# Optimization experiments

Hardware: AMD Instinct MI355X
Metric: run time of the kernel (lower is better)

The kernel has to match this reference:

```python
import jax, jax.numpy as jnp
import numpy as np

E = 8            # moe_num_experts
HIDDEN = 1024    # hidden_size
FFN = 4096       # ffn_hidden_size
TOKENS = 8192    # total tokens, pre-sorted by expert; balanced -> TOKENS // E per expert


def setup_inputs() -> dict:
    key = jax.random.key(0)
    k1, k2, k3 = jax.random.split(key, 3)
    x = jax.random.normal(k1, (TOKENS, HIDDEN), dtype=jnp.float32)
    # w1, w2 stored flattened as [E*FFN, HIDDEN], matching create_dmoe_expert_weights' view([-1, columns])
    w1 = jax.random.normal(k2, (E * FFN, HIDDEN), dtype=jnp.float32) * (1.0 / np.sqrt(HIDDEN))
    w2 = jax.random.normal(k3, (E * FFN, HIDDEN), dtype=jnp.float32) * (1.0 / np.sqrt(FFN))
    return {"x": x, "w1": w1, "w2": w2, "num_experts": E}


def reference(x, w1, w2, num_experts):
    # Block-diagonal topology of dMoE SparseMLP: tokens sorted by expert, each
    # expert owns a contiguous FFN slice of w1/w2. Equivalent grouped GEMM:
    #   out_e = gelu(x_e @ w1_e^T) @ w2_e   (megablocks gelu = tanh-approx GELU)
    tokens, hidden = x.shape
    ffn = w1.shape[0] // num_experts
    tpe = tokens // num_experts  # tokens per expert (balanced topology)
    xe = x.reshape(num_experts, tpe, hidden)        # [E, T/E, H]
    w1e = w1.reshape(num_experts, ffn, hidden)      # [E, F, H]
    w2e = w2.reshape(num_experts, ffn, hidden)      # [E, F, H]
    h = jax.nn.gelu(jnp.einsum('eth,efh->etf', xe, w1e), approximate=True)  # sdd + gelu
    out = jnp.einsum('etf,efh->eth', h, w2e)        # dsd
    return out.reshape(tokens, hidden)
```

## Files before the change

kernel.cpp:

```cpp
#include <hip/hip_runtime.h>
#include <hip/hip_bf16.h>
#include <stdint.h>

#define NE 8
#define HID 1024
#define FFN 4096
#define TOK 8192
#define TPE (TOK / NE)

typedef __attribute__((ext_vector_type(8))) short    bf16x8;
typedef __attribute__((ext_vector_type(4))) float    f32x4;
typedef __attribute__((ext_vector_type(4))) unsigned short ushort4v;
typedef __attribute__((ext_vector_type(8))) unsigned short ushort8v;


__device__ __forceinline__ unsigned short f2bf(float f) {
    union { float f; unsigned u; } c; c.f = f;
    unsigned r = c.u + 0x7fffu + ((c.u >> 16) & 1u);
    return (unsigned short)(r >> 16);
}

__device__ __forceinline__ float gelu_tanh(float x) {
    const float c0 = 0.7978845608028654f;
    const float c1 = 0.044715f;
    float u = c0 * (x + c1 * x * x * x);
    float t = 1.0f - 2.0f / (1.0f + __expf(2.0f * u));
    return 0.5f * x * (1.0f + t);
}

typedef const __attribute__((address_space(1))) void gbl_void_t;
typedef __attribute__((address_space(3))) void lds_void_t;

__device__ __forceinline__ void gload_lds16(const void* g, void* l) {
    __builtin_amdgcn_global_load_lds((gbl_void_t*)g, (lds_void_t*)l, 16, 0, 0);
}


__global__ void cvt_f32_bf16(const float* __restrict__ in,
                             unsigned short* __restrict__ out) {
    size_t i = ((size_t)blockIdx.x * blockDim.x + threadIdx.x) * 8;
    f32x4 a = *(const f32x4*)(in + i);
    f32x4 b = *(const f32x4*)(in + i + 4);
    ushort8v o;
#pragma unroll
    for (int j = 0; j < 4; j++) { o[j] = f2bf(a[j]); o[4 + j] = f2bf(b[j]); }
    *(ushort8v*)(out + i) = o;
}


__global__ void transpose_cvt(const float* __restrict__ in,
                              unsigned short* __restrict__ out) {
    __shared__ unsigned short tile[64][65];
    const int e  = blockIdx.z;
    const int f0 = blockIdx.x * 64;
    const int h0 = blockIdx.y * 64;
    const float*     src = in  + (size_t)e * FFN * HID;
    unsigned short*  dst = out + (size_t)e * HID * FFN;
    const int t  = threadIdx.x;
    const int tr = t >> 4;
    const int tc = (t & 15) * 4;
#pragma unroll
    for (int i = 0; i < 4; i++) {
        int f = i * 16 + tr;
        f32x4 v = *(const f32x4*)(src + (size_t)(f0 + f) * HID + h0 + tc);
#pragma unroll
        for (int j = 0; j < 4; j++) tile[f][tc + j] = f2bf(v[j]);
    }
    __syncthreads();
#pragma unroll
    for (int i = 0; i < 4; i++) {
        int h = i * 16 + tr;
        ushort4v o;
#pragma unroll
        for (int j = 0; j < 4; j++) o[j] = tile[tc + j][h];
        *(ushort4v*)(dst + (size_t)(h0 + h) * FFN + f0 + tc) = o;
    }
}


template <int BN, bool GELU>
__global__ __launch_bounds__(512, 2)
void gemm8p(const unsigned short* __restrict__ A,
            const unsigned short* __restrict__ B,
            void* __restrict__ Cout, int M, int N, int K) {
    constexpr int BM = 256, BK = 64;
    constexpr int NI = BN / 64;
    constexpr int NH = NI / 2;
    constexpr int ABYTES = BM * BK * 2;
    constexpr int BBYTES = BN * BK * 2;
    constexpr int BUF = ABYTES + BBYTES;
    constexpr int LPTA = ABYTES / (512 * 16);
    constexpr int LPTB = BBYTES / (512 * 16);
    constexpr int LPT = LPTA + LPTB;

    __shared__ __align__(16) char lds[2 * BUF];

    const int e  = blockIdx.z;
    const int m0 = blockIdx.x * BM;
    const int n0 = blockIdx.y * BN;
    const unsigned short* Ae = A + (size_t)e * M * K;
    const unsigned short* Be = B + (size_t)e * N * K;

    const int tid  = threadIdx.x;
    const int lane = tid & 63;
    const int w    = tid >> 6;
    const int wr   = w >> 2;
    const int wc   = w & 3;
    const int fr   = lane & 15;
    const int fq   = lane >> 4;
    const int swz  = (lane & 7) << 4;
    const int kx0  = (fq * 16) ^ swz;
    const int kx1  = (64 + fq * 16) ^ swz;
    const int aoff = (wr * 128 + fr) * 128;
    const int boff = ABYTES + (wc * (BN / 4) + fr) * 128;

    const unsigned short* asrc[LPTA];
    const unsigned short* bsrc[LPTB];
    int adst[LPTA], bdst[LPTB];
#pragma unroll
    for (int i = 0; i < LPTA; i++) {
        int c = tid + 512 * i; int row = c >> 3; int kb = (c & 7) << 4;
        int kbs = kb ^ ((row & 7) << 4);
        asrc[i] = Ae + (size_t)(m0 + row) * K + (kbs >> 1);
        adst[i] = c * 16;
    }
#pragma unroll
    for (int i = 0; i < LPTB; i++) {
        int c = tid + 512 * i; int row = c >> 3; int kb = (c & 7) << 4;
        int kbs = kb ^ ((row & 7) << 4);
        bsrc[i] = Be + (size_t)(n0 + row) * K + (kbs >> 1);
        bdst[i] = ABYTES + c * 16;
    }

    auto STAGE = [&](int it) {
        char* base = lds + (it & 1) * BUF;
        const int kt = it * BK;
#pragma unroll
        for (int i = 0; i < LPTA; i++) gload_lds16(asrc[i] + kt, base + adst[i]);
#pragma unroll
        for (int i = 0; i < LPTB; i++) gload_lds16(bsrc[i] + kt, base + bdst[i]);
    };

    f32x4 acc[8][NI];
#pragma unroll
    for (int i = 0; i < 8; i++)
#pragma unroll
        for (int j = 0; j < NI; j++) acc[i][j] = f32x4{0.f, 0.f, 0.f, 0.f};

    bf16x8 a[4][2], b[NH][2];
    const char* pa = nullptr; const char* pb = nullptr;

    auto LDA = [&](int mh) {
#pragma unroll
        for (int mi = 0; mi < 4; mi++) {
            a[mi][0] = *(const bf16x8*)(pa + mh * 8192 + mi * 2048 + kx0);
            a[mi][1] = *(const bf16x8*)(pa + mh * 8192 + mi * 2048 + kx1);
        }
    };
    auto LDB = [&](int nh) {
#pragma unroll
        for (int ni = 0; ni < NH; ni++) {
            b[ni][0] = *(const bf16x8*)(pb + nh * (NH * 2048) + ni * 2048 + kx0);
            b[ni][1] = *(const bf16x8*)(pb + nh * (NH * 2048) + ni * 2048 + kx1);
        }
    };
    auto MM = [&](int mh, int nh) {
        __builtin_amdgcn_s_setprio(1);
#pragma unroll
        for (int mi = 0; mi < 4; mi++)
#pragma unroll
            for (int ni = 0; ni < NH; ni++) {
                acc[mh * 4 + mi][nh * NH + ni] = __builtin_amdgcn_mfma_f32_16x16x32_bf16(
                    a[mi][0], b[ni][0], acc[mh * 4 + mi][nh * NH + ni], 0, 0, 0);
                acc[mh * 4 + mi][nh * NH + ni] = __builtin_amdgcn_mfma_f32_16x16x32_bf16(
                    a[mi][1], b[ni][1], acc[mh * 4 + mi][nh * NH + ni], 0, 0, 0);
            }
        __builtin_amdgcn_s_setprio(0);
    };

    STAGE(0); STAGE(1);
    if constexpr (LPT == 8) asm volatile("s_waitcnt vmcnt(8)" ::: "memory");
    else                    asm volatile("s_waitcnt vmcnt(6)" ::: "memory");
    __builtin_amdgcn_sched_barrier(0);
    __builtin_amdgcn_s_barrier();
    __builtin_amdgcn_sched_barrier(0);

    const int NT = K / BK;
    for (int it = 0; it < NT; ++it) {
        const char* bb = lds + (it & 1) * BUF;
        pa = bb + aoff; pb = bb + boff;
        LDA(0); LDB(0); MM(0, 0);
        LDB(1);         MM(0, 1);
        LDA(1);         MM(1, 1);
        LDB(0);         MM(1, 0);
        __builtin_amdgcn_sched_barrier(0);
        __builtin_amdgcn_s_barrier();
        __builtin_amdgcn_sched_barrier(0);
        if (it + 2 < NT) {
            STAGE(it + 2);
            if constexpr (LPT == 8) asm volatile("s_waitcnt vmcnt(8)" ::: "memory");
            else                    asm volatile("s_waitcnt vmcnt(6)" ::: "memory");
        } else {
            asm volatile("s_waitcnt vmcnt(0)" ::: "memory");
        }
        __builtin_amdgcn_sched_barrier(0);
        __builtin_amdgcn_s_barrier();
        __builtin_amdgcn_sched_barrier(0);
    }

    const int r0 = m0 + wr * 128 + fq * 4;
    const int c0 = n0 + wc * (BN / 4) + fr;
    if constexpr (GELU) {
        unsigned short* C = (unsigned short*)Cout + (size_t)e * M * N;
#pragma unroll
        for (int mi = 0; mi < 8; mi++)
#pragma unroll
            for (int ni = 0; ni < NI; ni++) {
                int row = r0 + mi * 16, col = c0 + ni * 16;
#pragma unroll
                for (int r = 0; r < 4; r++)
                    C[(size_t)(row + r) * N + col] = f2bf(gelu_tanh(acc[mi][ni][r]));
            }
    } else {
        float* C = (float*)Cout + (size_t)e * M * N;
#pragma unroll
        for (int mi = 0; mi < 8; mi++)
#pragma unroll
            for (int ni = 0; ni < NI; ni++) {
                int row = r0 + mi * 16, col = c0 + ni * 16;
#pragma unroll
                for (int r = 0; r < 4; r++)
                    C[(size_t)(row + r) * N + col] = acc[mi][ni][r];
            }
    }
}


__global__ void fused_fallback(const float* __restrict__ x,
                               const float* __restrict__ w1,
                               const float* __restrict__ w2,
                               float* __restrict__ out) {
    __shared__ float xs[HID];
    __shared__ float hs[FFN];
    const int tok = blockIdx.x;
    const int e   = tok / TPE;
    const float* w1e = w1 + (size_t)e * FFN * HID;
    const float* w2e = w2 + (size_t)e * FFN * HID;
    const int t = threadIdx.x;
    for (int i = t; i < HID; i += 256) xs[i] = x[(size_t)tok * HID + i];
    __syncthreads();
    for (int f = t; f < FFN; f += 256) {
        const float* wr = w1e + (size_t)f * HID;
        float s = 0.f;
        for (int k = 0; k < HID; k++) s += xs[k] * wr[k];
        hs[f] = gelu_tanh(s);
    }
    __syncthreads();
    for (int h = t; h < HID; h += 256) {
        float s = 0.f;
        for (int f = 0; f < FFN; f++) s += hs[f] * w2e[(size_t)f * HID + h];
        out[(size_t)tok * HID + h] = s;
    }
}


extern "C" void kernel_launch(void* const* d_in, const int* in_sizes, int n_in,
                              void* d_out, int out_size, void* d_ws, size_t ws_size,
                              hipStream_t stream) {
    const float* x  = (const float*)d_in[0];
    const float* w1 = (const float*)d_in[1];
    const float* w2 = (const float*)d_in[2];
    float* out = (float*)d_out;

    const size_t XB  = (size_t)TOK * HID * 2;
    const size_t W1B = (size_t)NE * FFN * HID * 2;
    const size_t W2B = W1B;
    const size_t HB  = (size_t)TOK * FFN * 2;
    const size_t need = XB + W1B + W2B + HB;

    if (ws_size >= need) {
        char* ws = (char*)d_ws;
        unsigned short* xb  = (unsigned short*)ws;
        unsigned short* w1b = (unsigned short*)(ws + XB);
        unsigned short* w2t = (unsigned short*)(ws + XB + W1B);
        unsigned short* hb  = (unsigned short*)(ws + XB + W1B + W2B);

        cvt_f32_bf16<<<(TOK * HID) / (256 * 8), 256, 0, stream>>>(x, xb);
        cvt_f32_bf16<<<(NE * FFN * HID) / (256 * 8), 256, 0, stream>>>(w1, w1b);
        transpose_cvt<<<dim3(FFN / 64, HID / 64, NE), 256, 0, stream>>>(w2, w2t);

        gemm8p<256, true><<<dim3(TPE / 256, FFN / 256, NE), 512, 0, stream>>>(
            xb, w1b, hb, TPE, FFN, HID);
        gemm8p<128, false><<<dim3(TPE / 256, HID / 128, NE), 512, 0, stream>>>(
            hb, w2t, out, TPE, HID, FFN);
    } else {
        fused_fallback<<<TOK, 256, 0, stream>>>(x, w1, w2, out);
    }
}
```

Baseline: 259.1 us.

## Interleave split global-to-LDS loads with quarter MFMA phases in 8-wave GEMM

```diff
diff --git a/kernel.cpp b/kernel.cpp
--- a/kernel.cpp
+++ b/kernel.cpp
@@ -84,62 +84,63 @@
             const unsigned short* __restrict__ B,
             void* __restrict__ Cout, int M, int N, int K) {
     constexpr int BM = 256, BK = 64;
-    constexpr int NI = BN / 64;
-    constexpr int NH = NI / 2;
+    constexpr int NH = BN / 128;
+    constexpr int NI = 2 * NH;
+    constexpr int LB = BN / 128;
+    constexpr int S  = BN / 8;
     constexpr int ABYTES = BM * BK * 2;
     constexpr int BBYTES = BN * BK * 2;
     constexpr int BUF = ABYTES + BBYTES;
-    constexpr int LPTA = ABYTES / (512 * 16);
-    constexpr int LPTB = BBYTES / (512 * 16);
-    constexpr int LPT = LPTA + LPTB;
+    constexpr int VMC = 2 + 2 * LB;
 
     __shared__ __align__(16) char lds[2 * BUF];
 
     const int e  = blockIdx.z;
     const int m0 = blockIdx.x * BM;
     const int n0 = blockIdx.y * BN;
-    const unsigned short* Ae = A + (size_t)e * M * K;
-    const unsigned short* Be = B + (size_t)e * N * K;
+    const size_t K2 = (size_t)K * 2;
+    const char* Ae = (const char*)(A + (size_t)e * M * K);
+    const char* Be = (const char*)(B + (size_t)e * N * K);
 
     const int tid  = threadIdx.x;
     const int lane = tid & 63;
     const int w    = tid >> 6;
-    const int wr   = w >> 2;
-    const int wc   = w & 3;
-    const int fr   = lane & 15;
-    const int fq   = lane >> 4;
-    const int swz  = (lane & 7) << 4;
-    const int kx0  = (fq * 16) ^ swz;
-    const int kx1  = (64 + fq * 16) ^ swz;
-    const int aoff = (wr * 128 + fr) * 128;
-    const int boff = ABYTES + (wc * (BN / 4) + fr) * 128;
-
-    const unsigned short* asrc[LPTA];
-    const unsigned short* bsrc[LPTB];
-    int adst[LPTA], bdst[LPTB];
-#pragma unroll
-    for (int i = 0; i < LPTA; i++) {
-        int c = tid + 512 * i; int row = c >> 3; int kb = (c & 7) << 4;
-        int kbs = kb ^ ((row & 7) << 4);
-        asrc[i] = Ae + (size_t)(m0 + row) * K + (kbs >> 1);
-        adst[i] = c * 16;
-    }
-#pragma unroll
-    for (int i = 0; i < LPTB; i++) {
-        int c = tid + 512 * i; int row = c >> 3; int kb = (c & 7) << 4;
-        int kbs = kb ^ ((row & 7) << 4);
-        bsrc[i] = Be + (size_t)(n0 + row) * K + (kbs >> 1);
-        bdst[i] = ABYTES + c * 16;
-    }
-
-    auto STAGE = [&](int it) {
-        char* base = lds + (it & 1) * BUF;
-        const int kt = it * BK;
-#pragma unroll
-        for (int i = 0; i < LPTA; i++) gload_lds16(asrc[i] + kt, base + adst[i]);
-#pragma unroll
-        for (int i = 0; i < LPTB; i++) gload_lds16(bsrc[i] + kt, base + bdst[i]);
-    };
+    const int wr   = w >> 2, wc = w & 3;
+    const int fr   = lane & 15, fq = lane >> 4;
+
+    const int rA  = tid >> 3;
+    const int kb  = (tid & 7) * 16;
+    const int kbs = kb ^ ((rA & 7) << 4);
+    const char* aptr = Ae + (size_t)(m0 + rA) * K2 + kbs;
+    const int   fB   = (rA / S) * 2 * S + (rA % S);
+    const char* bptr = Be + (size_t)(n0 + fB) * K2 + kbs;
+    char* dA0 = lds + rA * 128 + kb;
+    char* dA1 = dA0 + BUF;
+    char* dB0 = lds + ABYTES + fB * 128 + kb;
+    char* dB1 = dB0 + BUF;
+
+    auto SA = [&](int au, int kt, char* d) {
+        const char* s = aptr + (size_t)kt * 128;
+#pragma unroll
+        for (int i = 0; i < 2; i++)
+            gload_lds16(s + (size_t)(au * 64 + i * 128) * K2,
+                        d + (au * 64 + i * 128) * 128);
+    };
+    auto SB = [&](int bu, int kt, char* d) {
+        const char* s = bptr + (size_t)kt * 128;
+#pragma unroll
+        for (int i = 0; i < LB; i++)
+            gload_lds16(s + (size_t)(bu * S + i * 128) * K2,
+                        d + (bu * S + i * 128) * 128);
+    };
+
+    const int kx0 = (fq * 16) ^ ((lane & 7) << 4);
+    const char* paA = lds + (wr * 128 + fr) * 128;
+    const char* paB = lds + ABYTES + (wc * (BN / 4) + fr) * 128;
+    const char* pa0k0 = paA + kx0;        const char* pa0k1 = paA + (kx0 ^ 64);
+    const char* pa1k0 = pa0k0 + BUF;      const char* pa1k1 = pa0k1 + BUF;
+    const char* pb0k0 = paB + kx0;        const char* pb0k1 = paB + (kx0 ^ 64);
+    const char* pb1k0 = pb0k0 + BUF;      const char* pb1k1 = pb0k1 + BUF;
 
     f32x4 acc[8][NI];
 #pragma unroll
@@ -147,66 +148,77 @@
 #pragma unroll
         for (int j = 0; j < NI; j++) acc[i][j] = f32x4{0.f, 0.f, 0.f, 0.f};
 
-    bf16x8 a[4][2], b[NH][2];
-    const char* pa = nullptr; const char* pb = nullptr;
-
-    auto LDA = [&](int mh) {
+    bf16x8 a[4][2], b0[NH][2], b1[NH][2];
+
+    auto LDA = [&](const char* p0, const char* p1, int mq) {
 #pragma unroll
         for (int mi = 0; mi < 4; mi++) {
-            a[mi][0] = *(const bf16x8*)(pa + mh * 8192 + mi * 2048 + kx0);
-            a[mi][1] = *(const bf16x8*)(pa + mh * 8192 + mi * 2048 + kx1);
+            a[mi][0] = *(const bf16x8*)(p0 + mq * 8192 + mi * 2048);
+            a[mi][1] = *(const bf16x8*)(p1 + mq * 8192 + mi * 2048);
         }
     };
-    auto LDB = [&](int nh) {
+    auto LDB = [&](const char* p0, const char* p1, int nq, bf16x8 (&bb)[NH][2]) {
 #pragma unroll
         for (int ni = 0; ni < NH; ni++) {
-            b[ni][0] = *(const bf16x8*)(pb + nh * (NH * 2048) + ni * 2048 + kx0);
-            b[ni][1] = *(const bf16x8*)(pb + nh * (NH * 2048) + ni * 2048 + kx1);
+            bb[ni][0] = *(const bf16x8*)(p0 + (nq * (BN / 8) + ni * 16) * 128);
+            bb[ni][1] = *(const bf16x8*)(p1 + (nq * (BN / 8) + ni * 16) * 128);
         }
     };
-    auto MM = [&](int mh, int nh) {
+    auto MMQ = [&](int mq, int nq, bf16x8 (&bb)[NH][2]) {
         __builtin_amdgcn_s_setprio(1);
 #pragma unroll
         for (int mi = 0; mi < 4; mi++)
 #pragma unroll
             for (int ni = 0; ni < NH; ni++) {
-                acc[mh * 4 + mi][nh * NH + ni] = __builtin_amdgcn_mfma_f32_16x16x32_bf16(
-                    a[mi][0], b[ni][0], acc[mh * 4 + mi][nh * NH + ni], 0, 0, 0);
-                acc[mh * 4 + mi][nh * NH + ni] = __builtin_amdgcn_mfma_f32_16x16x32_bf16(
-                    a[mi][1], b[ni][1], acc[mh * 4 + mi][nh * NH + ni], 0, 0, 0);
+                f32x4& c = acc[mq * 4 + mi][nq * NH + ni];
+                c = __builtin_amdgcn_mfma_f32_16x16x32_bf16(a[mi][0], bb[ni][0], c, 0, 0, 0);
+                c = __builtin_amdgcn_mfma_f32_16x16x32_bf16(a[mi][1], bb[ni][1], c, 0, 0, 0);
             }
         __builtin_amdgcn_s_setprio(0);
     };
 
-    STAGE(0); STAGE(1);
-    if constexpr (LPT == 8) asm volatile("s_waitcnt vmcnt(8)" ::: "memory");
-    else                    asm volatile("s_waitcnt vmcnt(6)" ::: "memory");
-    __builtin_amdgcn_sched_barrier(0);
+#define BAR_LGKM()  __builtin_amdgcn_sched_barrier(0); __builtin_amdgcn_s_barrier(); \
+                    asm volatile("s_waitcnt lgkmcnt(0)" ::: "memory");               \
+                    __builtin_amdgcn_sched_barrier(0)
+#define EBAR()      __builtin_amdgcn_sched_barrier(0); __builtin_amdgcn_s_barrier(); \
+                    __builtin_amdgcn_sched_barrier(0)
+#define VMW()       asm volatile("s_waitcnt vmcnt(%0)" :: "n"(VMC) : "memory");      \
+                    __builtin_amdgcn_sched_barrier(0)
+
+    const int NT   = K / BK;
+    const int NTm1 = NT - 1;
+
+    SA(0, 0, dA0); SB(0, 0, dB0); SB(1, 0, dB0); SA(1, 0, dA0);
+    SA(0, 1, dA1); SB(0, 1, dB1); SB(1, 1, dB1);
+    VMW();
     __builtin_amdgcn_s_barrier();
     __builtin_amdgcn_sched_barrier(0);
 
-    const int NT = K / BK;
-    for (int it = 0; it < NT; ++it) {
-        const char* bb = lds + (it & 1) * BUF;
-        pa = bb + aoff; pb = bb + boff;
-        LDA(0); LDB(0); MM(0, 0);
-        LDB(1);         MM(0, 1);
-        LDA(1);         MM(1, 1);
-        LDB(0);         MM(1, 0);
-        __builtin_amdgcn_sched_barrier(0);
-        __builtin_amdgcn_s_barrier();
-        __builtin_amdgcn_sched_barrier(0);
-        if (it + 2 < NT) {
-            STAGE(it + 2);
-            if constexpr (LPT == 8) asm volatile("s_waitcnt vmcnt(8)" ::: "memory");
-            else                    asm volatile("s_waitcnt vmcnt(6)" ::: "memory");
-        } else {
-            asm volatile("s_waitcnt vmcnt(0)" ::: "memory");
-        }
-        __builtin_amdgcn_sched_barrier(0);
-        __builtin_amdgcn_s_barrier();
-        __builtin_amdgcn_sched_barrier(0);
-    }
+    const int NW = NT / 2;
+    for (int ww = 0; ww < NW; ++ww) {
+        const int T = 2 * ww;
+        const int kt1 = T + 1;
+        const int kt2 = (T + 2 < NT) ? T + 2 : NTm1;
+        const int kt3 = (T + 3 < NT) ? T + 3 : NTm1;
+
+        LDA(pa0k0, pa0k1, 0); LDB(pb0k0, pb0k1, 0, b0); SA(1, kt1, dA1);
+        BAR_LGKM(); MMQ(0, 0, b0); EBAR();
+        LDB(pb0k0, pb0k1, 1, b1); SA(0, kt2, dA0);
+        BAR_LGKM(); MMQ(0, 1, b1); EBAR();
+        LDA(pa0k0, pa0k1, 1); SB(0, kt2, dB0);
+        BAR_LGKM(); MMQ(1, 1, b1); EBAR();
+        SB(1, kt2, dB0);
+        BAR_LGKM(); MMQ(1, 0, b0); VMW(); EBAR();
+        LDA(pa1k0, pa1k1, 0); LDB(pb1k0, pb1k1, 0, b0); SA(1, kt2, dA0);
+        BAR_LGKM(); MMQ(0, 0, b0); EBAR();
+        LDB(pb1k0, pb1k1, 1, b1); SA(0, kt3, dA1);
+        BAR_LGKM(); MMQ(0, 1, b1); EBAR();
+        LDA(pa1k0, pa1k1, 1); SB(0, kt3, dB1);
+        BAR_LGKM(); MMQ(1, 1, b1); EBAR();
+        SB(1, kt3, dB1);
+        BAR_LGKM(); MMQ(1, 0, b0); VMW(); EBAR();
+    }
+    asm volatile("s_waitcnt vmcnt(0)" ::: "memory");
 
     const int r0 = m0 + wr * 128 + fq * 4;
     const int c0 = n0 + wc * (BN / 4) + fr;
@@ -233,6 +245,9 @@
                     C[(size_t)(row + r) * N + col] = acc[mi][ni][r];
             }
     }
+#undef BAR_LGKM
+#undef EBAR
+#undef VMW
 }
 
 
@@ -250,9 +265,9 @@
     for (int i = t; i < HID; i += 256) xs[i] = x[(size_t)tok * HID + i];
     __syncthreads();
     for (int f = t; f < FFN; f += 256) {
-        const float* wr = w1e + (size_t)f * HID;
+        const float* wr_ = w1e + (size_t)f * HID;
         float s = 0.f;
-        for (int k = 0; k < HID; k++) s += xs[k] * wr[k];
+        for (int k = 0; k < HID; k++) s += xs[k] * wr_[k];
         hs[f] = gelu_tanh(s);
     }
     __syncthreads();
```

Result: faster. 247.6 us (-4.4%).
